# Performance work log

Hardware: AMD Instinct MI355X
Metric: run time of the kernel (lower is better)

The kernel has to match this reference:

```python
import jax, jax.numpy as jnp
import numpy as np

DIM = 128
CODEBOOK_SIZE = 1024


def setup_inputs() -> dict:
    key = jax.random.key(0)
    kx, ke = jax.random.split(key)
    x = jax.random.normal(kx, (16, 4096, DIM), dtype=jnp.float32)
    # kaiming_uniform_ on (codebook_size, dim): bound = sqrt(6 / fan_in), fan_in = dim
    bound = float(np.sqrt(6.0 / DIM))
    embed = jax.random.uniform(ke, (CODEBOOK_SIZE, DIM), dtype=jnp.float32,
                               minval=-bound, maxval=bound)
    return {"x": x, "embed": embed}


def reference(x, embed):
    orig_shape = x.shape
    flat = x.reshape(-1, x.shape[-1])                     # [N, D]
    x2 = jnp.sum(flat * flat, axis=1, keepdims=True)      # [N, 1]
    e2 = jnp.sum(embed * embed, axis=1)                   # [K]
    dist = -(x2 - 2.0 * (flat @ embed.T) + e2[None, :])   # [N, K]
    embed_ind = jnp.argmax(dist, axis=-1)                 # [N]
    embed_ind = embed_ind.reshape(orig_shape[:-1])        # [B, S]
    quantize = jnp.take(embed, embed_ind, axis=0)         # [B, S, D]
    return quantize, embed_ind
```

## Files before the change

### kernel.cpp

```cpp
#include <hip/hip_runtime.h>

#define DIM     128
#define NCODES  1024
#define TILE_M  64
#define FLAGThr 0.018f
#define RPB     4
#define RGRID   1024

typedef __attribute__((ext_vector_type(8))) _Float16 half8;
typedef __attribute__((ext_vector_type(4))) _Float16 half4;
typedef __attribute__((ext_vector_type(4))) float    f32x4;

#define AS1 __attribute__((address_space(1)))
#define AS3 __attribute__((address_space(3)))


__global__ __launch_bounds__(256) void setup_kernel(
    const float* __restrict__ embed, double* __restrict__ e2d,
    float* __restrict__ e2f, _Float16* __restrict__ eh,
    float* __restrict__ embedT, int* __restrict__ cnt)
{
  __shared__ float tile[64][132];
  __shared__ double psum[4][64];
  if (blockIdx.x == 0 && threadIdx.x == 0) *cnt = 0;
  const int c0 = blockIdx.x * 64;
  const int t  = threadIdx.x;

  const f32x4* E4 = (const f32x4*)(embed + (size_t)c0 * DIM);
  #pragma unroll
  for (int i = 0; i < 8; ++i) {
    int e = t + i * 256;
    int r = e >> 5, c4 = e & 31;
    f32x4 v = E4[e];
    *(f32x4*)&tile[r][c4 * 4] = v;
    half4 h;
    h[0] = (_Float16)v[0]; h[1] = (_Float16)v[1];
    h[2] = (_Float16)v[2]; h[3] = (_Float16)v[3];
    *(half4*)&eh[(size_t)(c0 + r) * DIM + c4 * 4] = h;
  }
  __syncthreads();

  {
    int r = t & 63, part = t >> 6;
    double s = 0.0;
    #pragma unroll
    for (int k = 0; k < 32; ++k) {
      float v = tile[r][part * 32 + k];
      s += (double)v * v;
    }
    psum[part][r] = s;
  }
  __syncthreads();
  if (t < 64) {
    double s = psum[0][t] + psum[1][t] + psum[2][t] + psum[3][t];
    e2d[c0 + t] = s;
    e2f[c0 + t] = (float)s;
  }

  #pragma unroll
  for (int i = 0; i < 32; ++i) {
    int idx = t + i * 256;
    int k = idx >> 6, c = idx & 63;
    embedT[(size_t)k * NCODES + c0 + c] = tile[c][k];
  }
}

__global__ __launch_bounds__(256, 2) void pass1_kernel(
    const float* __restrict__ x, const float* __restrict__ embed,
    const _Float16* __restrict__ eh, const float* __restrict__ e2f,
    float* __restrict__ outQ, float* __restrict__ outIdx,
    int* __restrict__ cnt, int* __restrict__ list)
{
  __shared__ __align__(16) _Float16 xh[TILE_M * 136];
  __shared__ __align__(16) unsigned char bbuf[4][3][4096];
  __shared__ float rb_best[4][TILE_M];
  __shared__ float rb_sec [4][TILE_M];
  __shared__ int   fidx[TILE_M];

  const int tid  = threadIdx.x;
  const int row0 = blockIdx.x * TILE_M;
  const int l  = tid & 63, w = tid >> 6;
  const int rl = l & 15,  q = l >> 4;

#define STAGE_W(CH)                                                           \
  {                                                                           \
    const char* ebase = (const char*)eh + ((size_t)(CH) * 64 + w * 16) * 256; \
    unsigned char* buf = &bbuf[w][(CH) % 3][0];                               \
    _Pragma("unroll")                                                         \
    for (int j = 0; j < 4; ++j) {                                             \
      int u  = j * 64 + l;                   \
      int rr = u >> 4, cc = u & 15;                                           \
      const char* src = ebase + rr * 256 + ((cc ^ rr) * 16);                  \
      __builtin_amdgcn_global_load_lds(                                       \
          (AS1 void*)src,                                                     \
          (AS3 void*)(buf + j * 1024), 16, 0, 0);                             \
    }                                                                         \
  }

  float vin[16];
  #pragma unroll
  for (int g = 0; g < 16; ++g)
    vin[g] = fmaf(-0.5f, e2f[g * 64 + w * 16 + rl], -16.0f);

  {
    const f32x4* x4 = (const f32x4*)(x + (size_t)row0 * DIM);
    #pragma unroll
    for (int i = 0; i < 8; ++i) {
      int e = tid + i * 256;
      int r = e >> 5, c4 = e & 31;
      f32x4 v = x4[e];
      half4 h;
      h[0] = (_Float16)v[0]; h[1] = (_Float16)v[1];
      h[2] = (_Float16)v[2]; h[3] = (_Float16)v[3];
      *(half4*)&xh[r * 136 + c4 * 4] = h;
    }
  }
  __syncthreads();

  half8 afrag[4][4];
  #pragma unroll
  for (int m = 0; m < 4; ++m)
    #pragma unroll
    for (int ks = 0; ks < 4; ++ks)
      afrag[m][ks] = *(const half8*)&xh[(m * 16 + rl) * 136 + ks * 32 + q * 8];

  float bestp[16], secp[16];
  #pragma unroll
  for (int s = 0; s < 16; ++s) { bestp[s] = -3.0e38f; secp[s] = -3.3e38f; }

  STAGE_W(0)
  STAGE_W(1)
  STAGE_W(2)

  #pragma unroll
  for (int ch = 0; ch < 16; ++ch) {
    if (ch <= 13) {
      asm volatile("s_waitcnt vmcnt(8)" ::: "memory");
    } else if (ch == 14) {
      asm volatile("s_waitcnt vmcnt(4)" ::: "memory");
    } else {
      asm volatile("s_waitcnt vmcnt(0)" ::: "memory");
    }
    __builtin_amdgcn_sched_barrier(0);

    const unsigned char* bb = &bbuf[w][ch % 3][0];
    half8 bfrag[4];
    #pragma unroll
    for (int ks = 0; ks < 4; ++ks)
      bfrag[ks] = *(const half8*)(bb + rl * 256 + (((ks * 4 + q) ^ rl) * 16));

    const float vinit = vin[ch];
    const int mycode = ch * 64 + w * 16 + rl;
    #pragma unroll
    for (int m = 0; m < 4; ++m) {
      f32x4 acc = (f32x4){vinit, vinit, vinit, vinit};
      #pragma unroll
      for (int ks = 0; ks < 4; ++ks)
        acc = __builtin_amdgcn_mfma_f32_16x16x32_f16(afrag[m][ks], bfrag[ks], acc, 0, 0, 0);
      #pragma unroll
      for (int r = 0; r < 4; ++r) {
        const int s = m * 4 + r;
        float scp = __int_as_float((__float_as_int(acc[r]) & ~1023) | mycode);
        secp[s]  = __builtin_amdgcn_fmed3f(scp, bestp[s], secp[s]);
        bestp[s] = fmaxf(bestp[s], scp);
      }
    }

    if (ch + 3 < 16) {
      asm volatile("s_waitcnt lgkmcnt(0)" ::: "memory");
      __builtin_amdgcn_sched_barrier(0);
      STAGE_W(ch + 3)
    }
  }
#undef STAGE_W

  #pragma unroll
  for (int off = 1; off < 16; off <<= 1) {
    #pragma unroll
    for (int s = 0; s < 16; ++s) {
      float ob = __shfl_xor(bestp[s], off, 16);
      float os = __shfl_xor(secp[s],  off, 16);
      secp[s]  = fmaxf(__builtin_amdgcn_fmed3f(bestp[s], ob, secp[s]), os);
      bestp[s] = fmaxf(bestp[s], ob);
    }
  }
  if (rl == 0) {
    #pragma unroll
    for (int m = 0; m < 4; ++m)
      #pragma unroll
      for (int r = 0; r < 4; ++r) {
        int s = m * 4 + r;
        int row = m * 16 + q * 4 + r;
        rb_best[w][row] = bestp[s];
        rb_sec [w][row] = secp[s];
      }
  }
  __syncthreads();

  if (tid < TILE_M) {
    float bv = rb_best[0][tid], sv = rb_sec[0][tid];
    #pragma unroll
    for (int ww = 1; ww < 4; ++ww) {
      float ob = rb_best[ww][tid], os = rb_sec[ww][tid];
      sv = fmaxf(__builtin_amdgcn_fmed3f(bv, ob, sv), os);
      bv = fmaxf(bv, ob);
    }
    int bi = __float_as_int(bv) & 1023;
    int grow = row0 + tid;
    outIdx[grow] = (float)bi;
    fidx[tid] = bi;
    if (bv - sv <= FLAGThr) {
      int p = atomicAdd(cnt, 1);
      list[p] = grow;
    }
  }
  __syncthreads();

  {
    const f32x4* E4   = (const f32x4*)embed;
    f32x4*       out4 = (f32x4*)(outQ + (size_t)row0 * DIM);
    #pragma unroll
    for (int i = 0; i < 8; ++i) {
      int e = tid + i * 256;
      int r = e >> 5, c4 = e & 31;
      out4[e] = E4[fidx[r] * 32 + c4];
    }
  }
}

__global__ __launch_bounds__(256) void refine2_kernel(
    const float* __restrict__ x, const float* __restrict__ embed,
    const float* __restrict__ embedT,
    const double* __restrict__ e2d, const float* __restrict__ e2f,
    float* __restrict__ outQ, float* __restrict__ outIdx,
    const int* __restrict__ cnt, const int* __restrict__ list)
{
  __shared__ f32x4 xst[DIM];
  __shared__ float rb1[RPB][4], rb2[RPB][4];
  __shared__ int   ri1[RPB][4], ri2[RPB][4];
  __shared__ int   cand[RPB][2];

  const int t = threadIdx.x;
  const int l = t & 63, w = t >> 6;
  const int n = *cnt;
  float* xsf = (float*)xst;

  for (int base = blockIdx.x * RPB; base < n; base += RGRID * RPB) {
    const int nr = min(RPB, n - base);
    #pragma unroll
    for (int i = 0; i < 2; ++i) {
      int idx = t + i * 256;
      int r = idx >> 7, k = idx & 127;
      float v = 0.f;
      if (r < nr) v = x[(size_t)list[base + r] * DIM + k];
      xsf[k * RPB + r] = v;
    }
    __syncthreads();

    f32x4 dot[RPB];
    #pragma unroll
    for (int r = 0; r < RPB; ++r) dot[r] = (f32x4){0.f, 0.f, 0.f, 0.f};
    const f32x4* eT4 = (const f32x4*)embedT;
    #pragma unroll 4
    for (int k = 0; k < DIM; ++k) {
      f32x4 e4  = eT4[k * 256 + t];
      f32x4 xk4 = xst[k];
      #pragma unroll
      for (int r = 0; r < RPB; ++r) {
        dot[r][0] = fmaf(xk4[r], e4[0], dot[r][0]);
        dot[r][1] = fmaf(xk4[r], e4[1], dot[r][1]);
        dot[r][2] = fmaf(xk4[r], e4[2], dot[r][2]);
        dot[r][3] = fmaf(xk4[r], e4[3], dot[r][3]);
      }
    }

    #pragma unroll
    for (int r = 0; r < RPB; ++r) {
      float b1 = 3.4e38f, b2 = 3.4e38f; int i1 = 0, i2 = 0;
      #pragma unroll
      for (int j = 0; j < 4; ++j) {
        int c = 4 * t + j;
        float sc = fmaf(-2.0f, dot[r][j], e2f[c]);
        bool better = (sc < b1);
        float lv = better ? b1 : sc;  int li = better ? i1 : c;
        if (better) { b1 = sc; i1 = c; }
        bool t2 = (lv < b2) || (lv == b2 && li < i2);
        if (t2) { b2 = lv; i2 = li; }
      }
      #pragma unroll
      for (int off = 1; off < 64; off <<= 1) {
        float o1 = __shfl_xor(b1, off, 64); int oi1 = __shfl_xor(i1, off, 64);
        float o2 = __shfl_xor(b2, off, 64); int oi2 = __shfl_xor(i2, off, 64);
        bool take = (o1 < b1) || (o1 == b1 && oi1 < i1);
        float n1 = take ? o1 : b1; int ni1 = take ? oi1 : i1;
        float lo = take ? b1 : o1; int loi = take ? i1 : oi1;
        float c2v = take ? o2 : b2; int c2i = take ? oi2 : i2;
        bool u2 = (c2v < lo) || (c2v == lo && c2i < loi);
        b1 = n1; i1 = ni1;
        b2 = u2 ? c2v : lo; i2 = u2 ? c2i : loi;
      }
      if (l == 0) { rb1[r][w] = b1; ri1[r][w] = i1; rb2[r][w] = b2; ri2[r][w] = i2; }
    }
    __syncthreads();

    if (t < RPB) {
      float v1 = rb1[t][0], v2 = rb2[t][0]; int j1 = ri1[t][0], j2 = ri2[t][0];
      #pragma unroll
      for (int ww = 1; ww < 4; ++ww) {
        float o1 = rb1[t][ww], o2 = rb2[t][ww]; int oi1 = ri1[t][ww], oi2 = ri2[t][ww];
        bool take = (o1 < v1) || (o1 == v1 && oi1 < j1);
        float n1 = take ? o1 : v1; int ni1 = take ? oi1 : j1;
        float lo = take ? v1 : o1; int loi = take ? j1 : oi1;
        float c2v = take ? o2 : v2; int c2i = take ? oi2 : j2;
        bool u2 = (c2v < lo) || (c2v == lo && c2i < loi);
        v1 = n1; j1 = ni1; v2 = u2 ? c2v : lo; j2 = u2 ? c2i : loi;
      }
      cand[t][0] = j1; cand[t][1] = j2;
    }
    __syncthreads();

    if (w < nr) {
      int c1 = cand[w][0], c2 = cand[w][1];
      float xa = xsf[l * RPB + w], xb = xsf[(l + 64) * RPB + w];
      double p1 = (double)xa * (double)embed[(size_t)c1 * DIM + l]
                + (double)xb * (double)embed[(size_t)c1 * DIM + 64 + l];
      double p2 = (double)xa * (double)embed[(size_t)c2 * DIM + l]
                + (double)xb * (double)embed[(size_t)c2 * DIM + 64 + l];
      #pragma unroll
      for (int off = 1; off < 64; off <<= 1) {
        p1 += __shfl_xor(p1, off, 64);
        p2 += __shfl_xor(p2, off, 64);
      }
      double s1 = e2d[c1] - 2.0 * p1;
      double s2 = e2d[c2] - 2.0 * p2;
      int widx = ((s2 < s1) || (s2 == s1 && c2 < c1)) ? c2 : c1;
      int row = list[base + w];
      if (l == 0) outIdx[row] = (float)widx;
      outQ[(size_t)row * DIM + l]      = embed[(size_t)widx * DIM + l];
      outQ[(size_t)row * DIM + 64 + l] = embed[(size_t)widx * DIM + 64 + l];
    }
    __syncthreads();
  }
}

extern "C" void kernel_launch(void* const* d_in, const int* in_sizes, int n_in,
                              void* d_out, int out_size, void* d_ws, size_t ws_size,
                              hipStream_t stream) {
  const float* x     = (const float*)d_in[0];
  const float* embed = (const float*)d_in[1];
  const int N = in_sizes[0] / DIM;

  float* out    = (float*)d_out;
  float* outQ   = out;
  float* outIdx = out + (size_t)N * DIM;

  char* ws = (char*)d_ws;
  double*   e2d  = (double*)  (ws);
  float*    e2f  = (float*)   (ws + 8192);
  _Float16* eh   = (_Float16*)(ws + 12288);
  float*    eT   = (float*)   (ws + 274432);
  int*      cnt  = (int*)     (ws + 798720);
  int*      list = (int*)     (ws + 798976);

  setup_kernel  <<<NCODES / 64, 256, 0, stream>>>(embed, e2d, e2f, eh, eT, cnt);
  pass1_kernel  <<<N / TILE_M,  256, 0, stream>>>(x, embed, eh, e2f, outQ, outIdx, cnt, list);
  refine2_kernel<<<RGRID,       256, 0, stream>>>(x, embed, eT, e2d, e2f, outQ, outIdx, cnt, list);
}
```

Before: 134.5 us.

## Fuse setup, pass1 and refine into one cooperative persistent kernel

Replaces the three kernel launches with a single cooperative kernel of 512 blocks that runs setup, the MFMA coarse pass and the candidate refinement, separated by grid-wide syncs. Each block handles two 64-row tiles and overlaps its first x tile load with setup. Refinement now processes 8 rows per block instead of 4. It removes the launch gaps and tail effects between kernels, at the cost of grid-sync overhead, higher shared-memory use per block and a fixed grid size. The old three-kernel path is kept as a fallback if the cooperative launch fails.

```diff
diff --git a/kernel.cpp b/kernel.cpp
--- a/kernel.cpp
+++ b/kernel.cpp
@@ -1,11 +1,14 @@
 #include <hip/hip_runtime.h>
+#include <hip/hip_cooperative_groups.h>
+namespace cg = cooperative_groups;
 
 #define DIM     128
 #define NCODES  1024
 #define TILE_M  64
 #define FLAGThr 0.018f
 #define RPB     4
-#define RGRID   1024
+#define RPBF    8
+#define FGRID   512
 
 typedef __attribute__((ext_vector_type(8))) _Float16 half8;
 typedef __attribute__((ext_vector_type(4))) _Float16 half4;
@@ -14,6 +17,352 @@
 #define AS1 __attribute__((address_space(1)))
 #define AS3 __attribute__((address_space(3)))
 
+
+__global__ __launch_bounds__(256, 2) void fused_kernel(
+    const float* __restrict__ x, const float* __restrict__ embed,
+    double* __restrict__ e2d, float* __restrict__ e2f,
+    _Float16* __restrict__ eh, float* __restrict__ embedT,
+    float* __restrict__ outQ, float* __restrict__ outIdx,
+    int* __restrict__ cnt, int* __restrict__ list)
+{
+  __shared__ __align__(16) unsigned char smem[68864];
+  _Float16* xh = (_Float16*)smem;
+  float (*rb_best)[TILE_M] = (float (*)[TILE_M])(smem + 66560);
+  float (*rb_sec )[TILE_M] = (float (*)[TILE_M])(smem + 67584);
+  int*   fidx              = (int*)(smem + 68608);
+
+  const int tid = threadIdx.x, bid = blockIdx.x;
+  const int l = tid & 63, w = tid >> 6;
+  const int rl = l & 15,  q = l >> 4;
+
+  if (bid == 0 && tid == 0) *cnt = 0;
+
+  {
+    const f32x4* x4 = (const f32x4*)(x + (size_t)bid * TILE_M * DIM);
+    #pragma unroll
+    for (int i = 0; i < 8; ++i) {
+      int e = tid + i * 256;
+      int r = e >> 5, c4 = e & 31;
+      f32x4 v = x4[e];
+      half4 h;
+      h[0] = (_Float16)v[0]; h[1] = (_Float16)v[1];
+      h[2] = (_Float16)v[2]; h[3] = (_Float16)v[3];
+      *(half4*)&xh[r * 136 + c4 * 4] = h;
+    }
+  }
+
+  if (bid < 16) {
+    float  (*tile)[132] = (float  (*)[132])(smem + 17408);
+    double (*psum)[64]  = (double (*)[64]) (smem + 51200);
+    const int c0 = bid * 64;
+    const f32x4* E4 = (const f32x4*)(embed + (size_t)c0 * DIM);
+    #pragma unroll
+    for (int i = 0; i < 8; ++i) {
+      int e = tid + i * 256;
+      int r = e >> 5, c4 = e & 31;
+      f32x4 v = E4[e];
+      *(f32x4*)&tile[r][c4 * 4] = v;
+      half4 h;
+      h[0] = (_Float16)v[0]; h[1] = (_Float16)v[1];
+      h[2] = (_Float16)v[2]; h[3] = (_Float16)v[3];
+      *(half4*)&eh[(size_t)(c0 + r) * DIM + c4 * 4] = h;
+    }
+    __syncthreads();
+    {
+      int r = tid & 63, part = tid >> 6;
+      double s = 0.0;
+      #pragma unroll
+      for (int k = 0; k < 32; ++k) {
+        float v = tile[r][part * 32 + k];
+        s += (double)v * v;
+      }
+      psum[part][r] = s;
+    }
+    __syncthreads();
+    if (tid < 64) {
+      double s = psum[0][tid] + psum[1][tid] + psum[2][tid] + psum[3][tid];
+      e2d[c0 + tid] = s;
+      e2f[c0 + tid] = (float)s;
+    }
+    #pragma unroll
+    for (int i = 0; i < 32; ++i) {
+      int idx = tid + i * 256;
+      int k = idx >> 6, c = idx & 63;
+      embedT[(size_t)k * NCODES + c0 + c] = tile[c][k];
+    }
+  }
+
+  cg::this_grid().sync();
+
+#define STAGE_W(CH)                                                           \
+  {                                                                           \
+    const char* ebase = (const char*)eh + ((size_t)(CH) * 64 + w * 16) * 256; \
+    unsigned char* buf = smem + 17408 + (w * 3 + (CH) % 3) * 4096;            \
+    _Pragma("unroll")                                                         \
+    for (int j = 0; j < 4; ++j) {                                             \
+      int u  = j * 64 + l;                   \
+      int rr = u >> 4, cc = u & 15;                                           \
+      const char* src = ebase + rr * 256 + ((cc ^ rr) * 16);                  \
+      __builtin_amdgcn_global_load_lds(                                       \
+          (AS1 void*)src,                                                     \
+          (AS3 void*)(buf + j * 1024), 16, 0, 0);                             \
+    }                                                                         \
+  }
+
+  float vin[16];
+  #pragma unroll
+  for (int g = 0; g < 16; ++g)
+    vin[g] = fmaf(-0.5f, e2f[g * 64 + w * 16 + rl], -16.0f);
+  asm volatile("s_waitcnt vmcnt(0)" ::: "memory");
+  __builtin_amdgcn_sched_barrier(0);
+
+  for (int tt = 0; tt < 2; ++tt) {
+    const int row0 = (bid + tt * FGRID) * TILE_M;
+    if (tt) {
+      __syncthreads();
+      const f32x4* x4 = (const f32x4*)(x + (size_t)row0 * DIM);
+      #pragma unroll
+      for (int i = 0; i < 8; ++i) {
+        int e = tid + i * 256;
+        int r = e >> 5, c4 = e & 31;
+        f32x4 v = x4[e];
+        half4 h;
+        h[0] = (_Float16)v[0]; h[1] = (_Float16)v[1];
+        h[2] = (_Float16)v[2]; h[3] = (_Float16)v[3];
+        *(half4*)&xh[r * 136 + c4 * 4] = h;
+      }
+    }
+    __syncthreads();
+
+    half8 afrag[4][4];
+    #pragma unroll
+    for (int m = 0; m < 4; ++m)
+      #pragma unroll
+      for (int ks = 0; ks < 4; ++ks)
+        afrag[m][ks] = *(const half8*)&xh[(m * 16 + rl) * 136 + ks * 32 + q * 8];
+
+    float bestp[16], secp[16];
+    #pragma unroll
+    for (int s = 0; s < 16; ++s) { bestp[s] = -3.0e38f; secp[s] = -3.3e38f; }
+
+    STAGE_W(0)
+    STAGE_W(1)
+    STAGE_W(2)
+
+    #pragma unroll
+    for (int ch = 0; ch < 16; ++ch) {
+      if (ch <= 13) {
+        asm volatile("s_waitcnt vmcnt(8)" ::: "memory");
+      } else if (ch == 14) {
+        asm volatile("s_waitcnt vmcnt(4)" ::: "memory");
+      } else {
+        asm volatile("s_waitcnt vmcnt(0)" ::: "memory");
+      }
+      __builtin_amdgcn_sched_barrier(0);
+
+      const unsigned char* bb = smem + 17408 + (w * 3 + ch % 3) * 4096;
+      half8 bfrag[4];
+      #pragma unroll
+      for (int ks = 0; ks < 4; ++ks)
+        bfrag[ks] = *(const half8*)(bb + rl * 256 + (((ks * 4 + q) ^ rl) * 16));
+
+      const float vinit = vin[ch];
+      const int mycode = ch * 64 + w * 16 + rl;
+      #pragma unroll
+      for (int m = 0; m < 4; ++m) {
+        f32x4 acc = (f32x4){vinit, vinit, vinit, vinit};
+        #pragma unroll
+        for (int ks = 0; ks < 4; ++ks)
+          acc = __builtin_amdgcn_mfma_f32_16x16x32_f16(afrag[m][ks], bfrag[ks], acc, 0, 0, 0);
+        #pragma unroll
+        for (int r = 0; r < 4; ++r) {
+          const int s = m * 4 + r;
+          float scp = __int_as_float((__float_as_int(acc[r]) & ~1023) | mycode);
+          secp[s]  = __builtin_amdgcn_fmed3f(scp, bestp[s], secp[s]);
+          bestp[s] = fmaxf(bestp[s], scp);
+        }
+      }
+
+      if (ch + 3 < 16) {
+        asm volatile("s_waitcnt lgkmcnt(0)" ::: "memory");
+        __builtin_amdgcn_sched_barrier(0);
+        STAGE_W(ch + 3)
+      }
+    }
+
+    #pragma unroll
+    for (int off = 1; off < 16; off <<= 1) {
+      #pragma unroll
+      for (int s = 0; s < 16; ++s) {
+        float ob = __shfl_xor(bestp[s], off, 16);
+        float os = __shfl_xor(secp[s],  off, 16);
+        secp[s]  = fmaxf(__builtin_amdgcn_fmed3f(bestp[s], ob, secp[s]), os);
+        bestp[s] = fmaxf(bestp[s], ob);
+      }
+    }
+    if (rl == 0) {
+      #pragma unroll
+      for (int m = 0; m < 4; ++m)
+        #pragma unroll
+        for (int r = 0; r < 4; ++r) {
+          int s = m * 4 + r;
+          int row = m * 16 + q * 4 + r;
+          rb_best[w][row] = bestp[s];
+          rb_sec [w][row] = secp[s];
+        }
+    }
+    __syncthreads();
+
+    if (tid < TILE_M) {
+      float bv = rb_best[0][tid], sv = rb_sec[0][tid];
+      #pragma unroll
+      for (int ww = 1; ww < 4; ++ww) {
+        float ob = rb_best[ww][tid], os = rb_sec[ww][tid];
+        sv = fmaxf(__builtin_amdgcn_fmed3f(bv, ob, sv), os);
+        bv = fmaxf(bv, ob);
+      }
+      int bi = __float_as_int(bv) & 1023;
+      int grow = row0 + tid;
+      outIdx[grow] = (float)bi;
+      fidx[tid] = bi;
+      if (bv - sv <= FLAGThr) {
+        int p = atomicAdd(cnt, 1);
+        list[p] = grow;
+      }
+    }
+    __syncthreads();
+
+    {
+      const f32x4* E4   = (const f32x4*)embed;
+      f32x4*       out4 = (f32x4*)(outQ + (size_t)row0 * DIM);
+      #pragma unroll
+      for (int i = 0; i < 8; ++i) {
+        int e = tid + i * 256;
+        int r = e >> 5, c4 = e & 31;
+        out4[e] = E4[fidx[r] * 32 + c4];
+      }
+    }
+  }
+#undef STAGE_W
+
+  cg::this_grid().sync();
+
+  {
+    const int n = *cnt;
+    float* xsf = (float*)smem;
+    float (*rb1)[4]  = (float (*)[4])(smem + 17408);
+    float (*rb2)[4]  = (float (*)[4])(smem + 17536);
+    int   (*ri1)[4]  = (int   (*)[4])(smem + 17664);
+    int   (*ri2)[4]  = (int   (*)[4])(smem + 17792);
+    int   (*cand)[2] = (int   (*)[2])(smem + 17920);
+
+    for (int base = bid * RPBF; base < n; base += FGRID * RPBF) {
+      const int nr = min(RPBF, n - base);
+      #pragma unroll
+      for (int i = 0; i < 4; ++i) {
+        int idx = tid + i * 256;
+        int r = idx >> 7, k = idx & 127;
+        float v = 0.f;
+        if (r < nr) v = x[(size_t)list[base + r] * DIM + k];
+        xsf[k * RPBF + r] = v;
+      }
+      __syncthreads();
+
+      f32x4 dot[RPBF];
+      #pragma unroll
+      for (int r = 0; r < RPBF; ++r) dot[r] = (f32x4){0.f, 0.f, 0.f, 0.f};
+      const f32x4* eT4 = (const f32x4*)embedT;
+      #pragma unroll 4
+      for (int k = 0; k < DIM; ++k) {
+        f32x4 e4 = eT4[k * 256 + tid];
+        f32x4 xa = *(const f32x4*)&xsf[k * RPBF];
+        f32x4 xb = *(const f32x4*)&xsf[k * RPBF + 4];
+        #pragma unroll
+        for (int r = 0; r < 4; ++r) {
+          dot[r][0]   = fmaf(xa[r], e4[0], dot[r][0]);
+          dot[r][1]   = fmaf(xa[r], e4[1], dot[r][1]);
+          dot[r][2]   = fmaf(xa[r], e4[2], dot[r][2]);
+          dot[r][3]   = fmaf(xa[r], e4[3], dot[r][3]);
+          dot[r+4][0] = fmaf(xb[r], e4[0], dot[r+4][0]);
+          dot[r+4][1] = fmaf(xb[r], e4[1], dot[r+4][1]);
+          dot[r+4][2] = fmaf(xb[r], e4[2], dot[r+4][2]);
+          dot[r+4][3] = fmaf(xb[r], e4[3], dot[r+4][3]);
+        }
+      }
+
+      #pragma unroll
+      for (int r = 0; r < RPBF; ++r) {
+        float b1 = 3.4e38f, b2 = 3.4e38f; int i1 = 0, i2 = 0;
+        #pragma unroll
+        for (int j = 0; j < 4; ++j) {
+          int c = 4 * tid + j;
+          float sc = fmaf(-2.0f, dot[r][j], e2f[c]);
+          bool better = (sc < b1);
+          float lv = better ? b1 : sc;  int li = better ? i1 : c;
+          if (better) { b1 = sc; i1 = c; }
+          bool t2 = (lv < b2) || (lv == b2 && li < i2);
+          if (t2) { b2 = lv; i2 = li; }
+        }
+        #pragma unroll
+        for (int off = 1; off < 64; off <<= 1) {
+          float o1 = __shfl_xor(b1, off, 64); int oi1 = __shfl_xor(i1, off, 64);
+          float o2 = __shfl_xor(b2, off, 64); int oi2 = __shfl_xor(i2, off, 64);
+          bool take = (o1 < b1) || (o1 == b1 && oi1 < i1);
+          float n1 = take ? o1 : b1; int ni1 = take ? oi1 : i1;
+          float lo = take ? b1 : o1; int loi = take ? i1 : oi1;
+          float c2v = take ? o2 : b2; int c2i = take ? oi2 : i2;
+          bool u2 = (c2v < lo) || (c2v == lo && c2i < loi);
+          b1 = n1; i1 = ni1;
+          b2 = u2 ? c2v : lo; i2 = u2 ? c2i : loi;
+        }
+        if (l == 0) { rb1[r][w] = b1; ri1[r][w] = i1; rb2[r][w] = b2; ri2[r][w] = i2; }
+      }
+      __syncthreads();
+
+      if (tid < RPBF) {
+        float v1 = rb1[tid][0], v2 = rb2[tid][0]; int j1 = ri1[tid][0], j2 = ri2[tid][0];
+        #pragma unroll
+        for (int ww = 1; ww < 4; ++ww) {
+          float o1 = rb1[tid][ww], o2 = rb2[tid][ww]; int oi1 = ri1[tid][ww], oi2 = ri2[tid][ww];
+          bool take = (o1 < v1) || (o1 == v1 && oi1 < j1);
+          float n1 = take ? o1 : v1; int ni1 = take ? oi1 : j1;
+          float lo = take ? v1 : o1; int loi = take ? j1 : oi1;
+          float c2v = take ? o2 : v2; int c2i = take ? oi2 : j2;
+          bool u2 = (c2v < lo) || (c2v == lo && c2i < loi);
+          v1 = n1; j1 = ni1; v2 = u2 ? c2v : lo; j2 = u2 ? c2i : loi;
+        }
+        cand[tid][0] = j1; cand[tid][1] = j2;
+      }
+      __syncthreads();
+
+      #pragma unroll
+      for (int rr0 = 0; rr0 < 2; ++rr0) {
+        const int rr = w + rr0 * 4;
+        if (rr < nr) {
+          int c1 = cand[rr][0], c2 = cand[rr][1];
+          float xa = xsf[l * RPBF + rr], xb = xsf[(l + 64) * RPBF + rr];
+          double p1 = (double)xa * (double)embed[(size_t)c1 * DIM + l]
+                    + (double)xb * (double)embed[(size_t)c1 * DIM + 64 + l];
+          double p2 = (double)xa * (double)embed[(size_t)c2 * DIM + l]
+                    + (double)xb * (double)embed[(size_t)c2 * DIM + 64 + l];
+          #pragma unroll
+          for (int off = 1; off < 64; off <<= 1) {
+            p1 += __shfl_xor(p1, off, 64);
+            p2 += __shfl_xor(p2, off, 64);
+          }
+          double s1 = e2d[c1] - 2.0 * p1;
+          double s2 = e2d[c2] - 2.0 * p2;
+          int widx = ((s2 < s1) || (s2 == s1 && c2 < c1)) ? c2 : c1;
+          int row = list[base + rr];
+          if (l == 0) outIdx[row] = (float)widx;
+          outQ[(size_t)row * DIM + l]      = embed[(size_t)widx * DIM + l];
+          outQ[(size_t)row * DIM + 64 + l] = embed[(size_t)widx * DIM + 64 + l];
+        }
+      }
+      __syncthreads();
+    }
+  }
+}
 
 __global__ __launch_bounds__(256) void setup_kernel(
     const float* __restrict__ embed, double* __restrict__ e2d,
@@ -39,7 +388,6 @@
     *(half4*)&eh[(size_t)(c0 + r) * DIM + c4 * 4] = h;
   }
   __syncthreads();
-
   {
     int r = t & 63, part = t >> 6;
     double s = 0.0;
@@ -56,7 +404,6 @@
     e2d[c0 + t] = s;
     e2f[c0 + t] = (float)s;
   }
-
   #pragma unroll
   for (int i = 0; i < 32; ++i) {
     int idx = t + i * 256;
@@ -88,7 +435,7 @@
     unsigned char* buf = &bbuf[w][(CH) % 3][0];                               \
     _Pragma("unroll")                                                         \
     for (int j = 0; j < 4; ++j) {                                             \
-      int u  = j * 64 + l;                   \
+      int u  = j * 64 + l;                                                    \
       int rr = u >> 4, cc = u & 15;                                           \
       const char* src = ebase + rr * 256 + ((cc ^ rr) * 16);                  \
       __builtin_amdgcn_global_load_lds(                                       \
@@ -245,7 +592,7 @@
   const int n = *cnt;
   float* xsf = (float*)xst;
 
-  for (int base = blockIdx.x * RPB; base < n; base += RGRID * RPB) {
+  for (int base = blockIdx.x * RPB; base < n; base += 1024 * RPB) {
     const int nr = min(RPB, n - base);
     #pragma unroll
     for (int i = 0; i < 2; ++i) {
@@ -362,7 +709,15 @@
   int*      cnt  = (int*)     (ws + 798720);
   int*      list = (int*)     (ws + 798976);
 
-  setup_kernel  <<<NCODES / 64, 256, 0, stream>>>(embed, e2d, e2f, eh, eT, cnt);
-  pass1_kernel  <<<N / TILE_M,  256, 0, stream>>>(x, embed, eh, e2f, outQ, outIdx, cnt, list);
-  refine2_kernel<<<RGRID,       256, 0, stream>>>(x, embed, eT, e2d, e2f, outQ, outIdx, cnt, list);
+  void* args[] = { (void*)&x, (void*)&embed, (void*)&e2d, (void*)&e2f,
+                   (void*)&eh, (void*)&eT, (void*)&outQ, (void*)&outIdx,
+                   (void*)&cnt, (void*)&list };
+  hipError_t err = hipLaunchCooperativeKernel((const void*)fused_kernel,
+                                              dim3(FGRID), dim3(256),
+                                              args, 0, stream);
+  if (err != hipSuccess) {
+    setup_kernel  <<<NCODES / 64, 256, 0, stream>>>(embed, e2d, e2f, eh, eT, cnt);
+    pass1_kernel  <<<N / TILE_M,  256, 0, stream>>>(x, embed, eh, e2f, outQ, outIdx, cnt, list);
+    refine2_kernel<<<1024,        256, 0, stream>>>(x, embed, eT, e2d, e2f, outQ, outIdx, cnt, list);
+  }
 }
```

After: 320.4 us. 2.38x slower.

## Add fp16 residual split for x to tighten scores and lower refinement threshold

Applied to the files above, without the earlier changes.

The x tile is split into a high fp16 part and a low fp16 residual, and the residual is also fed through MFMA, so the scores carry near-fp32 precision for x. The packed-index trick now keeps only 4 low mantissa bits (the chunk id) instead of 10, and the full code id is rebuilt and reduced explicitly with tie-breaking. With the more accurate scores the ambiguity threshold drops from 0.018 to 0.005, so fewer rows get flagged for the exact second-pass refinement. The cost is twice the MFMA work in pass1, an extra global reload of x, more registers, and a slower reduction in exchange for a cheaper refinement pass.

```diff
diff --git a/kernel.cpp b/kernel.cpp
--- a/kernel.cpp
+++ b/kernel.cpp
@@ -3,7 +3,7 @@
 #define DIM     128
 #define NCODES  1024
 #define TILE_M  64
-#define FLAGThr 0.018f
+#define FLAGThr 0.005f
 #define RPB     4
 #define RGRID   1024
 
@@ -75,6 +75,7 @@
   __shared__ __align__(16) unsigned char bbuf[4][3][4096];
   __shared__ float rb_best[4][TILE_M];
   __shared__ float rb_sec [4][TILE_M];
+  __shared__ int   rb_bidx[4][TILE_M];
   __shared__ int   fidx[TILE_M];
 
   const int tid  = threadIdx.x;
@@ -124,9 +125,33 @@
     for (int ks = 0; ks < 4; ++ks)
       afrag[m][ks] = *(const half8*)&xh[(m * 16 + rl) * 136 + ks * 32 + q * 8];
 
+  half8 alo[4][4];
+  #pragma unroll
+  for (int m = 0; m < 4; ++m)
+    #pragma unroll
+    for (int ks = 0; ks < 4; ++ks) {
+      const float* xp = x + (size_t)(row0 + m * 16 + rl) * DIM + ks * 32 + q * 8;
+      f32x4 a = *(const f32x4*)xp;
+      f32x4 b = *(const f32x4*)(xp + 4);
+      half8 h = afrag[m][ks];
+      half8 lo;
+      lo[0] = (_Float16)(a[0] - (float)h[0]);
+      lo[1] = (_Float16)(a[1] - (float)h[1]);
+      lo[2] = (_Float16)(a[2] - (float)h[2]);
+      lo[3] = (_Float16)(a[3] - (float)h[3]);
+      lo[4] = (_Float16)(b[0] - (float)h[4]);
+      lo[5] = (_Float16)(b[1] - (float)h[5]);
+      lo[6] = (_Float16)(b[2] - (float)h[6]);
+      lo[7] = (_Float16)(b[3] - (float)h[7]);
+      alo[m][ks] = lo;
+    }
+
   float bestp[16], secp[16];
   #pragma unroll
   for (int s = 0; s < 16; ++s) { bestp[s] = -3.0e38f; secp[s] = -3.3e38f; }
+
+  asm volatile("s_waitcnt vmcnt(0)" ::: "memory");
+  __builtin_amdgcn_sched_barrier(0);
 
   STAGE_W(0)
   STAGE_W(1)
@@ -150,17 +175,19 @@
       bfrag[ks] = *(const half8*)(bb + rl * 256 + (((ks * 4 + q) ^ rl) * 16));
 
     const float vinit = vin[ch];
-    const int mycode = ch * 64 + w * 16 + rl;
     #pragma unroll
     for (int m = 0; m < 4; ++m) {
       f32x4 acc = (f32x4){vinit, vinit, vinit, vinit};
       #pragma unroll
       for (int ks = 0; ks < 4; ++ks)
+        acc = __builtin_amdgcn_mfma_f32_16x16x32_f16(alo[m][ks], bfrag[ks], acc, 0, 0, 0);
+      #pragma unroll
+      for (int ks = 0; ks < 4; ++ks)
         acc = __builtin_amdgcn_mfma_f32_16x16x32_f16(afrag[m][ks], bfrag[ks], acc, 0, 0, 0);
       #pragma unroll
       for (int r = 0; r < 4; ++r) {
         const int s = m * 4 + r;
-        float scp = __int_as_float((__float_as_int(acc[r]) & ~1023) | mycode);
+        float scp = __int_as_float((__float_as_int(acc[r]) & ~15) | ch);
         secp[s]  = __builtin_amdgcn_fmed3f(scp, bestp[s], secp[s]);
         bestp[s] = fmaxf(bestp[s], scp);
       }
@@ -174,14 +201,28 @@
   }
 #undef STAGE_W
 
+  float bval[16], sval[16];
+  int   bcode[16];
+  #pragma unroll
+  for (int s = 0; s < 16; ++s) {
+    int bi = __float_as_int(bestp[s]);
+    bval[s]  = __int_as_float(bi & ~15);
+    bcode[s] = (bi & 15) * 64 + w * 16 + rl;
+    sval[s]  = __int_as_float(__float_as_int(secp[s]) & ~15);
+  }
   #pragma unroll
   for (int off = 1; off < 16; off <<= 1) {
     #pragma unroll
     for (int s = 0; s < 16; ++s) {
-      float ob = __shfl_xor(bestp[s], off, 16);
-      float os = __shfl_xor(secp[s],  off, 16);
-      secp[s]  = fmaxf(__builtin_amdgcn_fmed3f(bestp[s], ob, secp[s]), os);
-      bestp[s] = fmaxf(bestp[s], ob);
+      float ov = __shfl_xor(bval[s],  off, 16);
+      int   oc = __shfl_xor(bcode[s], off, 16);
+      float os = __shfl_xor(sval[s],  off, 16);
+      bool take = (ov > bval[s]) || (ov == bval[s] && oc < bcode[s]);
+      float lose = take ? bval[s] : ov;
+      float cs   = take ? os : sval[s];
+      bval[s]  = take ? ov : bval[s];
+      bcode[s] = take ? oc : bcode[s];
+      sval[s]  = fmaxf(cs, lose);
     }
   }
   if (rl == 0) {
@@ -191,24 +232,28 @@
       for (int r = 0; r < 4; ++r) {
         int s = m * 4 + r;
         int row = m * 16 + q * 4 + r;
-        rb_best[w][row] = bestp[s];
-        rb_sec [w][row] = secp[s];
+        rb_best[w][row] = bval[s];
+        rb_bidx[w][row] = bcode[s];
+        rb_sec [w][row] = sval[s];
       }
   }
   __syncthreads();
 
   if (tid < TILE_M) {
-    float bv = rb_best[0][tid], sv = rb_sec[0][tid];
+    float bv = rb_best[0][tid]; int bc = rb_bidx[0][tid]; float sv = rb_sec[0][tid];
     #pragma unroll
     for (int ww = 1; ww < 4; ++ww) {
-      float ob = rb_best[ww][tid], os = rb_sec[ww][tid];
-      sv = fmaxf(__builtin_amdgcn_fmed3f(bv, ob, sv), os);
-      bv = fmaxf(bv, ob);
-    }
-    int bi = __float_as_int(bv) & 1023;
+      float ob = rb_best[ww][tid]; int oc = rb_bidx[ww][tid]; float os = rb_sec[ww][tid];
+      bool take = (ob > bv) || (ob == bv && oc < bc);
+      float lose = take ? bv : ob;
+      float cs   = take ? os : sv;
+      bv = take ? ob : bv;
+      bc = take ? oc : bc;
+      sv = fmaxf(cs, lose);
+    }
     int grow = row0 + tid;
-    outIdx[grow] = (float)bi;
-    fidx[tid] = bi;
+    outIdx[grow] = (float)bc;
+    fidx[tid] = bc;
     if (bv - sv <= FLAGThr) {
       int p = atomicAdd(cnt, 1);
       list[p] = grow;
```

Result: slower. 309.0 us (+129.7%).
